# Optimization experiments

Measured on AMD Instinct MI355X. Metric: run time of the kernel, lower is better.

## Reference

```python
import jax, jax.numpy as jnp
import numpy as np

N_NODES = 50000
N_EDGES = 800000
N_GRAPHS = 500
DIM = 64
RBF_DIM = 5      # ceil(cutoff/width) = ceil(5.0/1)
N_CONV = 3
N_TYPES = 100
CLS_DIM = 2000
CUTOFF = 5.0

def _w(key, shape, fan_in):
    return jax.random.normal(key, shape, dtype=jnp.float32) / np.sqrt(fan_in)

def setup_inputs() -> dict:
    key = jax.random.key(0)
    ks = jax.random.split(key, 16)
    return {
        "node_types": jax.random.randint(ks[0], (N_NODES,), 0, N_TYPES, dtype=jnp.int32),
        "edge_src": jax.random.randint(ks[1], (N_EDGES,), 0, N_NODES, dtype=jnp.int32),
        "edge_dst": jax.random.randint(ks[2], (N_EDGES,), 0, N_NODES, dtype=jnp.int32),
        "graph_ids": jnp.sort(jax.random.randint(ks[3], (N_NODES,), 0, N_GRAPHS, dtype=jnp.int32)),
        "distance": jax.random.uniform(ks[4], (N_EDGES,), dtype=jnp.float32) * CUTOFF,
        "emb": jax.random.normal(ks[5], (N_TYPES, DIM), dtype=jnp.float32),
        "conv_w1": _w(ks[6], (N_CONV, DIM, DIM), DIM),
        "cf1_w": _w(ks[7], (N_CONV, RBF_DIM, DIM), RBF_DIM),
        "cf1_b": jnp.zeros((N_CONV, DIM), jnp.float32),
        "cf2_w": _w(ks[8], (N_CONV, DIM, DIM), DIM),
        "cf2_b": jnp.zeros((N_CONV, DIM), jnp.float32),
        "nl2_w": _w(ks[9], (N_CONV, DIM, DIM), DIM),
        "nl2_b": jnp.zeros((N_CONV, DIM), jnp.float32),
        "nl3_w": _w(ks[10], (N_CONV, DIM, DIM), DIM),
        "nl3_b": jnp.zeros((N_CONV, DIM), jnp.float32),
        "d1_w": _w(ks[11], (DIM, 256), DIM),
        "d1_b": jnp.zeros((256,), jnp.float32),
        "d2_w": _w(ks[12], (256, 256), 256),
        "d2_b": jnp.zeros((256,), jnp.float32),
        "cls_w": _w(ks[13], (256, CLS_DIM), 256),
        "cls_b": jnp.zeros((CLS_DIM,), jnp.float32),
        "ac_w": _w(ks[14], (256, N_TYPES), 256),
        "ac_b": jnp.zeros((N_TYPES,), jnp.float32),
    }

def _sp2(x):
    # torch nn.Softplus(beta=0.5): (1/0.5) * log(1 + exp(0.5 * x))
    return 2.0 * jax.nn.softplus(0.5 * x)

def reference(node_types, edge_src, edge_dst, graph_ids, distance, emb,
              conv_w1, cf1_w, cf1_b, cf2_w, cf2_b, nl2_w, nl2_b, nl3_w, nl3_b,
              d1_w, d1_b, d2_w, d2_b, cls_w, cls_b, ac_w, ac_b):
    # RBF expansion of edge distances: centers = linspace(low, high, n_centers)
    centers = jnp.linspace(0.0, CUTOFF, RBF_DIM)
    gap = centers[1] - centers[0]
    rbf = jnp.exp(-(1.0 / gap) * (distance[:, None] - centers) ** 2)  # [E, RBF_DIM]

    node = emb[node_types]                                            # AtomEmbedding -> [N, D]
    for i in range(N_CONV):                                           # Interaction layers
        new_node = node @ conv_w1[i]                                  # Linear(dim, dim, bias=False)
        eh = _sp2(rbf @ cf1_w[i] + cf1_b[i])                          # CFConv filter network
        eh = _sp2(eh @ cf2_w[i] + cf2_b[i])                           # [E, D]
        msg = new_node[edge_src] * eh                                 # fn.u_mul_e gather
        agg = jax.ops.segment_sum(msg, edge_dst, num_segments=N_NODES)  # fn.sum scatter
        t = _sp2(agg @ nl2_w[i] + nl2_b[i])
        node = node + t @ nl3_w[i] + nl3_b[i]                         # residual update

    atom = node @ d1_w + d1_b
    atom = jax.nn.softplus(atom) - jnp.log(2.0)                       # ShiftSoftplus
    res = atom @ d2_w + d2_b                                          # [N, 256]
    atoms_preds = jax.nn.relu(res) @ ac_w + ac_b                      # [N, 100]

    ones = jnp.ones((N_NODES,), jnp.float32)
    counts = jax.ops.segment_sum(ones, graph_ids, num_segments=N_GRAPHS)
    emb_g = jax.ops.segment_sum(res, graph_ids, num_segments=N_GRAPHS) / jnp.maximum(counts, 1.0)[:, None]
    cls_preds = emb_g @ cls_w + cls_b                                 # [B, cls_dim]
    return atoms_preds, cls_preds
```

## Files before the change

kernel.cpp:

```cpp
#include <hip/hip_runtime.h>
#include <math.h>

#define N_NODES 50000
#define N_EDGES 800000
#define N_GRAPHS 500
#define DIM 64
#define RBF_DIM 5
#define N_CONV 3
#define CLS_DIM 2000
#define ACT_DIM 100
#define HID 256
#define TAB 256
#define TABP (TAB - 1)
#define CAP 64

typedef __attribute__((ext_vector_type(8))) short bf16x8;
typedef __attribute__((ext_vector_type(4))) float f32x4;
#define MFMA16(a,b,c) __builtin_amdgcn_mfma_f32_16x16x32_bf16(a,b,c,0,0,0)

__device__ __forceinline__ float sp2f(float x){
    float y = 0.5f * x;
    return 2.0f * (fmaxf(y, 0.0f) + __logf(1.0f + __expf(-fabsf(y))));
}
__device__ __forceinline__ float sspf(float x){
    return fmaxf(x, 0.0f) + __logf(1.0f + __expf(-fabsf(x))) - 0.69314718055994531f;
}
__device__ __forceinline__ short f2b(float x){
    union { float f; unsigned u; } v; v.f = x;
    unsigned r = v.u + 0x7FFFu + ((v.u >> 16) & 1u);
    return (short)(r >> 16);
}
__device__ __forceinline__ float b2f(short x){
    union { unsigned u; float f; } v; v.u = ((unsigned)(unsigned short)x) << 16;
    return v.f;
}

__global__ void k_tw(const float* __restrict__ cw, const float* __restrict__ n2,
                     const float* __restrict__ n3, const float* __restrict__ d1w,
                     const float* __restrict__ d2w, const float* __restrict__ acw,
                     const float* __restrict__ clsw, const float* __restrict__ emb,
                     short* __restrict__ cwt, short* __restrict__ n2t, short* __restrict__ n3t,
                     short* __restrict__ d1t, short* __restrict__ d2t, short* __restrict__ act,
                     short* __restrict__ clswt, short* __restrict__ embw0b){
    int b = blockIdx.x, tid = threadIdx.x;
    if (b < 144){
        int i = b * 256 + tid;
        int y = i >> 12, j = i & 4095;
        int which = y / 3, layer = y % 3;
        const float* src = (which == 0 ? cw : which == 1 ? n2 : n3) + layer * 4096;
        short* dst = (which == 0 ? cwt : which == 1 ? n2t : n3t) + layer * 4096;
        int k = j >> 6, n = j & 63;
        dst[n * 64 + k] = f2b(src[k * 64 + n]);
    } else if (b < 208){
        int i = (b - 144) * 256 + tid;
        int k = i >> 8, n = i & 255;
        d1t[n * 64 + k] = f2b(d1w[k * 256 + n]);
    } else if (b < 464){
        int i = (b - 208) * 256 + tid;
        int k = i >> 8, n = i & 255;
        d2t[n * 256 + k] = f2b(d2w[k * 256 + n]);
    } else if (b < 576){
        int i = (b - 464) * 256 + tid;
        int n = i >> 8, k = i & 255;
        act[n * 256 + k] = f2b(n < ACT_DIM ? acw[k * ACT_DIM + n] : 0.f);
    } else if (b < 2624){
        int i = (b - 576) * 256 + tid;
        int k = i >> 11, n = i & 2047;
        clswt[n * 256 + k] = f2b(n < CLS_DIM ? clsw[k * CLS_DIM + n] : 0.f);
    } else {
        int i = (b - 2624) * 256 + tid;
        if (i < 100 * 64){
            int t = i >> 6, c = i & 63;
            float a = 0.f;
            #pragma unroll 8
            for (int k = 0; k < 64; ++k) a += emb[t * 64 + k] * cw[k * 64 + c];
            embw0b[i] = f2b(a);
        }
    }
}

__global__ void k_embed(const int* __restrict__ types, const float* __restrict__ emb,
                        const short* __restrict__ embw0b,
                        float* __restrict__ node, short* __restrict__ nodeb,
                        short* __restrict__ nnb,
                        const int* __restrict__ gid, float* __restrict__ counts){
    int i = blockIdx.x * 256 + threadIdx.x;
    if (i < N_NODES * DIM){
        int t = types[i >> 6], c = i & 63;
        float v = emb[t * 64 + c];
        node[i] = v; nodeb[i] = f2b(v);
        nnb[i] = embw0b[t * 64 + c];
    }
    if (i < N_NODES) atomicAdd(&counts[gid[i]], 1.0f);
}

__global__ void k_scat(const int* __restrict__ esrc, const int* __restrict__ edst,
                       const float* __restrict__ dist,
                       int* __restrict__ cnt, unsigned* __restrict__ edata){
    int e = blockIdx.x * 256 + threadIdx.x;
    if (e >= N_EDGES) return;
    int d = edst[e];
    int pos = atomicAdd(&cnt[d], 1);
    if (pos < CAP){
        const float SC16 = (float)(TAB - 1) * 16.0f / 5.0f;
        int v = (int)(dist[e] * SC16 + 0.5f);
        v = min(v, (TAB - 1) * 16);
        edata[d * CAP + pos] = ((unsigned)v << 17) | (unsigned)esrc[e];
    }
}

__global__ __launch_bounds__(256) void k_table3(const float* __restrict__ cf1w_all,
    const float* __restrict__ cf1b_all, const float* __restrict__ cf2w_all,
    const float* __restrict__ cf2b_all, unsigned* __restrict__ tabp_all)
{
    int L = blockIdx.y;
    const float* cf1w = cf1w_all + L * RBF_DIM * DIM;
    const float* cf1b = cf1b_all + L * DIM;
    const float* cf2w = cf2w_all + L * DIM * DIM;
    const float* cf2b = cf2b_all + L * DIM;
    unsigned short* tp = (unsigned short*)(tabp_all + L * TABP * 64);
    __shared__ float s_cf1[RBF_DIM * 64];
    __shared__ float s_cf1b[64], s_cf2b[64];
    __shared__ float s_cf2[64 * 64];
    __shared__ float s_h1[4 * 64];
    int tid = threadIdx.x;
    int c = tid & 63, g = tid >> 6;
    for (int i = tid; i < 64 * 64; i += 256) s_cf2[i] = cf2w[i];
    for (int i = tid; i < RBF_DIM * 64; i += 256) s_cf1[i] = cf1w[i];
    if (tid < 64){ s_cf1b[tid] = cf1b[tid]; s_cf2b[tid] = cf2b[tid]; }
    __syncthreads();
    int entry = blockIdx.x * 4 + g;
    float d = (float)entry * (5.0f / (float)(TAB - 1));
    {
        float acc = s_cf1b[c];
        #pragma unroll
        for (int j = 0; j < RBF_DIM; ++j){
            float t = d - 1.25f * (float)j;
            acc += __expf(-0.8f * t * t) * s_cf1[j * 64 + c];
        }
        s_h1[g * 64 + c] = sp2f(acc);
    }
    __syncthreads();
    {
        float acc = s_cf2b[c];
        #pragma unroll 8
        for (int k = 0; k < 64; ++k) acc += s_h1[g * 64 + k] * s_cf2[k * 64 + c];
        unsigned short h = (unsigned short)f2b(sp2f(acc));
        if (entry < TABP) tp[(entry * 64 + c) * 2] = h;
        if (entry > 0)    tp[((entry - 1) * 64 + c) * 2 + 1] = h;
    }
}

__global__ __launch_bounds__(256) void k_agg(const unsigned* __restrict__ edata,
    const int* __restrict__ cnt, const unsigned* __restrict__ tabp,
    const short* __restrict__ nnb, short* __restrict__ aggb)
{
    int tid = threadIdx.x;
    int c = tid & 63, r = tid >> 6;
    int n = blockIdx.x * 4 + r;
    if (n >= N_NODES) return;
    int m = min(cnt[n], CAP);
    unsigned ev = (c < m) ? edata[n * CAP + c] : 0u;
    int s_l = (int)(ev & 0x1FFFFu);
    int v_l = (int)(ev >> 17);
    int i0_l = min(v_l >> 4, TAB - 2);
    float f_l = (float)(v_l - (i0_l << 4)) * 0.0625f;
    int pk_l = (i0_l << 17) | s_l;
    float acc = 0.f;
    int e = 0;
    for (; e + 8 <= m; e += 8){
        int p[8]; float f[8];
        #pragma unroll
        for (int j = 0; j < 8; ++j){ p[j] = __shfl(pk_l, e + j); f[j] = __shfl(f_l, e + j); }
        unsigned u[8]; float nn[8];
        #pragma unroll
        for (int j = 0; j < 8; ++j){
            u[j]  = tabp[(p[j] >> 17) * 64 + c];
            nn[j] = b2f(nnb[(p[j] & 0x1FFFF) * 64 + c]);
        }
        #pragma unroll
        for (int j = 0; j < 8; ++j){
            float w0 = __uint_as_float(u[j] << 16);
            float w1 = __uint_as_float(u[j] & 0xffff0000u);
            acc += nn[j] * (w0 + (w1 - w0) * f[j]);
        }
    }
    for (; e + 4 <= m; e += 4){
        int p[4]; float f[4];
        #pragma unroll
        for (int j = 0; j < 4; ++j){ p[j] = __shfl(pk_l, e + j); f[j] = __shfl(f_l, e + j); }
        unsigned u[4]; float nn[4];
        #pragma unroll
        for (int j = 0; j < 4; ++j){
            u[j]  = tabp[(p[j] >> 17) * 64 + c];
            nn[j] = b2f(nnb[(p[j] & 0x1FFFF) * 64 + c]);
        }
        #pragma unroll
        for (int j = 0; j < 4; ++j){
            float w0 = __uint_as_float(u[j] << 16);
            float w1 = __uint_as_float(u[j] & 0xffff0000u);
            acc += nn[j] * (w0 + (w1 - w0) * f[j]);
        }
    }
    for (; e < m; ++e){
        int   p = __shfl(pk_l, e); float f = __shfl(f_l, e);
        int i0 = p >> 17, s = p & 0x1FFFF;
        unsigned u = tabp[i0 * 64 + c];
        float w0 = __uint_as_float(u << 16), w1 = __uint_as_float(u & 0xffff0000u);
        acc += b2f(nnb[s * 64 + c]) * (w0 + (w1 - w0) * f);
    }
    aggb[n * 64 + c] = f2b(acc);
}

__global__ __launch_bounds__(256) void k_update(const short* __restrict__ aggb,
    const short* __restrict__ nl2t, const float* __restrict__ nl2b,
    const short* __restrict__ nl3t, const float* __restrict__ nl3b,
    float* __restrict__ node, short* __restrict__ nodeb,
    const short* __restrict__ wnext, short* __restrict__ nnb)
{
    __shared__ short sT[32 * 80];
    int tid = threadIdx.x, wave = tid >> 6, lane = tid & 63;
    int quad = lane >> 4, l16 = lane & 15;
    int row0 = blockIdx.x * 32;
    int rt = wave >> 1;
    int ctb = (wave & 1) * 2;
    f32x4 acc[2] = {{0,0,0,0},{0,0,0,0}};
    #pragma unroll
    for (int kt = 0; kt < 2; ++kt){
        int k0 = kt * 32 + quad * 8;
        int rw = row0 + rt * 16 + l16;
        bf16x8 a = (rw < N_NODES) ? *(const bf16x8*)&aggb[rw * 64 + k0] : (bf16x8){0,0,0,0,0,0,0,0};
        #pragma unroll
        for (int i = 0; i < 2; ++i){
            bf16x8 b = *(const bf16x8*)&nl2t[((ctb + i) * 16 + l16) * 64 + k0];
            acc[i] = MFMA16(a, b, acc[i]);
        }
    }
    #pragma unroll
    for (int i = 0; i < 2; ++i)
        #pragma unroll
        for (int reg = 0; reg < 4; ++reg){
            int rl = rt * 16 + quad * 4 + reg;
            int col = (ctb + i) * 16 + l16;
            sT[rl * 80 + col] = f2b(sp2f(acc[i][reg] + nl2b[col]));
        }
    __syncthreads();
    f32x4 acc2[2] = {{0,0,0,0},{0,0,0,0}};
    #pragma unroll
    for (int kt = 0; kt < 2; ++kt){
        int k0 = kt * 32 + quad * 8;
        bf16x8 a = *(const bf16x8*)&sT[(rt * 16 + l16) * 80 + k0];
        #pragma unroll
        for (int i = 0; i < 2; ++i){
            bf16x8 b = *(const bf16x8*)&nl3t[((ctb + i) * 16 + l16) * 64 + k0];
            acc2[i] = MFMA16(a, b, acc2[i]);
        }
    }
    short vb[2][4];
    #pragma unroll
    for (int i = 0; i < 2; ++i)
        #pragma unroll
        for (int reg = 0; reg < 4; ++reg){
            int row = row0 + rt * 16 + quad * 4 + reg;
            int col = (ctb + i) * 16 + l16;
            float v = 0.f;
            if (row < N_NODES){
                v = node[row * 64 + col] + acc2[i][reg] + nl3b[col];
                node[row * 64 + col] = v;
            }
            short vbs = f2b(v);
            vb[i][reg] = vbs;
            if (row < N_NODES) nodeb[row * 64 + col] = vbs;
        }
    if (wnext){
        __syncthreads();
        #pragma unroll
        for (int i = 0; i < 2; ++i)
            #pragma unroll
            for (int reg = 0; reg < 4; ++reg)
                sT[(rt * 16 + quad * 4 + reg) * 80 + (ctb + i) * 16 + l16] = vb[i][reg];
        __syncthreads();
        f32x4 acc3[2] = {{0,0,0,0},{0,0,0,0}};
        #pragma unroll
        for (int kt = 0; kt < 2; ++kt){
            int k0 = kt * 32 + quad * 8;
            bf16x8 a = *(const bf16x8*)&sT[(rt * 16 + l16) * 80 + k0];
            #pragma unroll
            for (int i = 0; i < 2; ++i){
                bf16x8 b = *(const bf16x8*)&wnext[((ctb + i) * 16 + l16) * 64 + k0];
                acc3[i] = MFMA16(a, b, acc3[i]);
            }
        }
        #pragma unroll
        for (int i = 0; i < 2; ++i)
            #pragma unroll
            for (int reg = 0; reg < 4; ++reg){
                int row = row0 + rt * 16 + quad * 4 + reg;
                int col = (ctb + i) * 16 + l16;
                if (row < N_NODES) nnb[row * 64 + col] = f2b(acc3[i][reg]);
            }
    }
}

__global__ __launch_bounds__(256) void k_r123(const short* __restrict__ nodeb,
    const short* __restrict__ d1t, const float* __restrict__ d1b,
    const short* __restrict__ d2t, const float* __restrict__ d2b_,
    const short* __restrict__ act, const float* __restrict__ acb,
    const int* __restrict__ gid, float* __restrict__ gacc,
    float* __restrict__ out_atoms)
{
    __shared__ short satom[32 * 264];
    int tid = threadIdx.x, wave = tid >> 6, lane = tid & 63;
    int quad = lane >> 4, l16 = lane & 15;
    int row0 = blockIdx.x * 32;
    {
        f32x4 acc[2][4] = {{{0,0,0,0},{0,0,0,0},{0,0,0,0},{0,0,0,0}},
                           {{0,0,0,0},{0,0,0,0},{0,0,0,0},{0,0,0,0}}};
        #pragma unroll
        for (int kt = 0; kt < 2; ++kt){
            int k0 = kt * 32 + quad * 8;
            bf16x8 a[2];
            #pragma unroll
            for (int rt = 0; rt < 2; ++rt){
                int rw = row0 + rt * 16 + l16;
                a[rt] = (rw < N_NODES) ? *(const bf16x8*)&nodeb[rw * 64 + k0] : (bf16x8){0,0,0,0,0,0,0,0};
            }
            #pragma unroll
            for (int ct = 0; ct < 4; ++ct){
                bf16x8 b = *(const bf16x8*)&d1t[(wave * 64 + ct * 16 + l16) * 64 + k0];
                #pragma unroll
                for (int rt = 0; rt < 2; ++rt) acc[rt][ct] = MFMA16(a[rt], b, acc[rt][ct]);
            }
        }
        #pragma unroll
        for (int rt = 0; rt < 2; ++rt)
            #pragma unroll
            for (int ct = 0; ct < 4; ++ct){
                int col = wave * 64 + ct * 16 + l16;
                float bb = d1b[col];
                #pragma unroll
                for (int reg = 0; reg < 4; ++reg)
                    satom[(rt * 16 + quad * 4 + reg) * 264 + col] = f2b(sspf(acc[rt][ct][reg] + bb));
            }
    }
    __syncthreads();
    f32x4 acc2[2][4] = {{{0,0,0,0},{0,0,0,0},{0,0,0,0},{0,0,0,0}},
                        {{0,0,0,0},{0,0,0,0},{0,0,0,0},{0,0,0,0}}};
    for (int kt = 0; kt < 8; ++kt){
        int k0 = kt * 32 + quad * 8;
        bf16x8 a[2];
        #pragma unroll
        for (int rt = 0; rt < 2; ++rt)
            a[rt] = *(const bf16x8*)&satom[(rt * 16 + l16) * 264 + k0];
        #pragma unroll
        for (int ct = 0; ct < 4; ++ct){
            bf16x8 b = *(const bf16x8*)&d2t[(wave * 64 + ct * 16 + l16) * HID + k0];
            #pragma unroll
            for (int rt = 0; rt < 2; ++rt) acc2[rt][ct] = MFMA16(a[rt], b, acc2[rt][ct]);
        }
    }
    __syncthreads();
    #pragma unroll
    for (int rt = 0; rt < 2; ++rt)
        #pragma unroll
        for (int ct = 0; ct < 4; ++ct){
            int col = wave * 64 + ct * 16 + l16;
            float bb = d2b_[col];
            #pragma unroll
            for (int reg = 0; reg < 4; ++reg)
                satom[(rt * 16 + quad * 4 + reg) * 264 + col] = f2b(acc2[rt][ct][reg] + bb);
        }
    __syncthreads();
    {
        float run[4] = {0.f, 0.f, 0.f, 0.f};
        int   cur[4] = {-1, -1, -1, -1};
        for (int r = 0; r < 8; ++r){
            #pragma unroll
            for (int ch = 0; ch < 4; ++ch){
                int row = ch * 8 + r;
                int n = row0 + row;
                if (n >= N_NODES) continue;
                short s = satom[row * 264 + tid];
                float v = b2f(s);
                int g = gid[n];
                if (g != cur[ch]){
                    if (cur[ch] >= 0) atomicAdd(&gacc[cur[ch] * HID + tid], run[ch]);
                    run[ch] = 0.f; cur[ch] = g;
                }
                run[ch] += v;
                satom[row * 264 + tid] = (v > 0.f) ? s : (short)0;
            }
        }
        #pragma unroll
        for (int ch = 0; ch < 4; ++ch)
            if (cur[ch] >= 0) atomicAdd(&gacc[cur[ch] * HID + tid], run[ch]);
    }
    __syncthreads();
    {
        int nct = (wave < 3) ? 2 : 1;
        f32x4 acc3[2][2] = {{{0,0,0,0},{0,0,0,0}},{{0,0,0,0},{0,0,0,0}}};
        for (int kt = 0; kt < 8; ++kt){
            int k0 = kt * 32 + quad * 8;
            bf16x8 a[2];
            #pragma unroll
            for (int rt = 0; rt < 2; ++rt)
                a[rt] = *(const bf16x8*)&satom[(rt * 16 + l16) * 264 + k0];
            for (int j = 0; j < nct; ++j){
                int ct = wave + j * 4;
                bf16x8 b = *(const bf16x8*)&act[(ct * 16 + l16) * HID + k0];
                #pragma unroll
                for (int rt = 0; rt < 2; ++rt) acc3[rt][j] = MFMA16(a[rt], b, acc3[rt][j]);
            }
        }
        #pragma unroll
        for (int rt = 0; rt < 2; ++rt)
            for (int j = 0; j < nct; ++j){
                int col = (wave + j * 4) * 16 + l16;
                if (col >= ACT_DIM) continue;
                float bb = acb[col];
                #pragma unroll
                for (int reg = 0; reg < 4; ++reg){
                    int row = row0 + rt * 16 + quad * 4 + reg;
                    if (row < N_NODES) out_atoms[row * ACT_DIM + col] = acc3[rt][j][reg] + bb;
                }
            }
    }
}

__global__ void k_embg(const float* __restrict__ gacc, const float* __restrict__ counts,
                       short* __restrict__ gclsb){
    int i = blockIdx.x * 256 + threadIdx.x;
    if (i < N_GRAPHS * HID){
        int g = i >> 8;
        gclsb[i] = f2b(gacc[i] / fmaxf(counts[g], 1.0f));
    }
}

__global__ __launch_bounds__(256) void k_cls2(const short* __restrict__ gclsb,
    const short* __restrict__ clswt, const float* __restrict__ clsb,
    float* __restrict__ out_cls)
{
    int tid = threadIdx.x, wave = tid >> 6, lane = tid & 63;
    int quad = lane >> 4, l16 = lane & 15;
    int row0 = blockIdx.x * 32;
    int colbase = blockIdx.y * 256 + wave * 64;
    f32x4 acc[2][4] = {{{0,0,0,0},{0,0,0,0},{0,0,0,0},{0,0,0,0}},
                       {{0,0,0,0},{0,0,0,0},{0,0,0,0},{0,0,0,0}}};
    for (int kt = 0; kt < 8; ++kt){
        int k0 = kt * 32 + quad * 8;
        bf16x8 a[2];
        #pragma unroll
        for (int rt = 0; rt < 2; ++rt){
            int rw = row0 + rt * 16 + l16;
            a[rt] = (rw < N_GRAPHS) ? *(const bf16x8*)&gclsb[rw * HID + k0] : (bf16x8){0,0,0,0,0,0,0,0};
        }
        #pragma unroll
        for (int ct = 0; ct < 4; ++ct){
            bf16x8 b = *(const bf16x8*)&clswt[(colbase + ct * 16 + l16) * HID + k0];
            #pragma unroll
            for (int rt = 0; rt < 2; ++rt) acc[rt][ct] = MFMA16(a[rt], b, acc[rt][ct]);
        }
    }
    #pragma unroll
    for (int rt = 0; rt < 2; ++rt)
        #pragma unroll
        for (int ct = 0; ct < 4; ++ct){
            int col = colbase + ct * 16 + l16;
            if (col >= CLS_DIM) continue;
            float bb = clsb[col];
            #pragma unroll
            for (int reg = 0; reg < 4; ++reg){
                int row = row0 + rt * 16 + quad * 4 + reg;
                if (row < N_GRAPHS) out_cls[row * CLS_DIM + col] = acc[rt][ct][reg] + bb;
            }
        }
}

extern "C" void kernel_launch(void* const* d_in, const int* in_sizes, int n_in,
                              void* d_out, int out_size, void* d_ws, size_t ws_size,
                              hipStream_t stream)
{
    const int*   node_types = (const int*)d_in[0];
    const int*   edge_src   = (const int*)d_in[1];
    const int*   edge_dst   = (const int*)d_in[2];
    const int*   graph_ids  = (const int*)d_in[3];
    const float* distance   = (const float*)d_in[4];
    const float* emb        = (const float*)d_in[5];
    const float* conv_w1    = (const float*)d_in[6];
    const float* cf1_w      = (const float*)d_in[7];
    const float* cf1_b      = (const float*)d_in[8];
    const float* cf2_w      = (const float*)d_in[9];
    const float* cf2_b      = (const float*)d_in[10];
    const float* nl2_w      = (const float*)d_in[11];
    const float* nl2_b      = (const float*)d_in[12];
    const float* nl3_w      = (const float*)d_in[13];
    const float* nl3_b      = (const float*)d_in[14];
    const float* d1_w       = (const float*)d_in[15];
    const float* d1_b       = (const float*)d_in[16];
    const float* d2_w       = (const float*)d_in[17];
    const float* d2_b       = (const float*)d_in[18];
    const float* cls_w      = (const float*)d_in[19];
    const float* cls_b      = (const float*)d_in[20];
    const float* ac_w       = (const float*)d_in[21];
    const float* ac_b       = (const float*)d_in[22];

    float*    gacc   = (float*)d_ws;
    float*    counts = gacc + 128000;
    int*      cnt    = (int*)(counts + 512);
    short*    nodeb  = (short*)(cnt + 50048);
    short*    nnb    = nodeb + 3200000;
    short*    aggb   = nnb + 3200000;
    unsigned* tabp   = (unsigned*)(aggb + 3200000);
    short*    cw1t   = (short*)(tabp + 3 * 16320);
    short*    n2t    = cw1t + 12288;
    short*    n3t    = n2t + 12288;
    short*    d1t    = n3t + 12288;
    short*    d2t    = d1t + 16384;
    short*    act    = d2t + 65536;
    short*    clswt  = act + 28672;
    short*    gclsb  = clswt + 524288;
    short*    embw0b = gclsb + 128000;
    float*    node   = (float*)(embw0b + 6400);
    unsigned* edata  = (unsigned*)(node + 3200000);
    float*    out    = (float*)d_out;

    (void)hipMemsetAsync(gacc, 0, (128000 + 512) * sizeof(float) + 50048 * sizeof(int), stream);

    k_tw<<<2649, 256, 0, stream>>>(conv_w1, nl2_w, nl3_w, d1_w, d2_w, ac_w, cls_w, emb,
                                   cw1t, n2t, n3t, d1t, d2t, act, clswt, embw0b);
    k_table3<<<dim3(TAB / 4, 3), 256, 0, stream>>>(cf1_w, cf1_b, cf2_w, cf2_b, tabp);

    k_embed<<<(N_NODES * DIM + 255) / 256, 256, 0, stream>>>(node_types, emb, embw0b,
        node, nodeb, nnb, graph_ids, counts);
    k_scat<<<(N_EDGES + 255) / 256, 256, 0, stream>>>(edge_src, edge_dst, distance,
                                                      cnt, edata);

    for (int i = 0; i < N_CONV; ++i){
        k_agg<<<(N_NODES + 3) / 4, 256, 0, stream>>>(edata, cnt, tabp + i * TABP * 64,
                                                     nnb, aggb);
        k_update<<<(N_NODES + 31) / 32, 256, 0, stream>>>(aggb,
            n2t + i * 4096, nl2_b + i * DIM, n3t + i * 4096, nl3_b + i * DIM,
            node, nodeb, (i < N_CONV - 1) ? (cw1t + (i + 1) * 4096) : (const short*)nullptr, nnb);
    }

    k_r123<<<(N_NODES + 31) / 32, 256, 0, stream>>>(nodeb, d1t, d1_b, d2t, d2_b,
                                                    act, ac_b, graph_ids, gacc, out);
    k_embg<<<(N_GRAPHS * HID + 255) / 256, 256, 0, stream>>>(gacc, counts, gclsb);
    k_cls2<<<dim3((N_GRAPHS + 31) / 32, (CLS_DIM + 255) / 256), 256, 0, stream>>>(
        gclsb, clswt, cls_b, out + N_NODES * ACT_DIM);
}
```

Measured before the change: 429.5 us.

## Fuse edge aggregation into node update kernel with ping-pong node buffers

Merges the per-node gather/aggregate kernel into the MFMA update kernel. Each 256-thread block now aggregates 32 nodes, with each wave handling 8 nodes one after another, and stages the bf16 aggregates in shared memory instead of a global buffer. The projected node features are double-buffered so the next layer's inputs are not overwritten while other blocks still read them. This removes a launch per layer and the global write and read of the aggregate array. In exchange, each wave now handles nodes serially, which reduces the parallelism available for hiding the latency of the random gather.

New measurement: 432.0 us. About the same (+0.6%).

```diff
diff --git a/kernel.cpp b/kernel.cpp
--- a/kernel.cpp
+++ b/kernel.cpp
@@ -151,85 +151,83 @@
     }
 }
 
-__global__ __launch_bounds__(256) void k_agg(const unsigned* __restrict__ edata,
+__global__ __launch_bounds__(256) void k_conv(const unsigned* __restrict__ edata,
     const int* __restrict__ cnt, const unsigned* __restrict__ tabp,
-    const short* __restrict__ nnb, short* __restrict__ aggb)
-{
-    int tid = threadIdx.x;
-    int c = tid & 63, r = tid >> 6;
-    int n = blockIdx.x * 4 + r;
-    if (n >= N_NODES) return;
-    int m = min(cnt[n], CAP);
-    unsigned ev = (c < m) ? edata[n * CAP + c] : 0u;
-    int s_l = (int)(ev & 0x1FFFFu);
-    int v_l = (int)(ev >> 17);
-    int i0_l = min(v_l >> 4, TAB - 2);
-    float f_l = (float)(v_l - (i0_l << 4)) * 0.0625f;
-    int pk_l = (i0_l << 17) | s_l;
-    float acc = 0.f;
-    int e = 0;
-    for (; e + 8 <= m; e += 8){
-        int p[8]; float f[8];
-        #pragma unroll
-        for (int j = 0; j < 8; ++j){ p[j] = __shfl(pk_l, e + j); f[j] = __shfl(f_l, e + j); }
-        unsigned u[8]; float nn[8];
-        #pragma unroll
-        for (int j = 0; j < 8; ++j){
-            u[j]  = tabp[(p[j] >> 17) * 64 + c];
-            nn[j] = b2f(nnb[(p[j] & 0x1FFFF) * 64 + c]);
-        }
-        #pragma unroll
-        for (int j = 0; j < 8; ++j){
-            float w0 = __uint_as_float(u[j] << 16);
-            float w1 = __uint_as_float(u[j] & 0xffff0000u);
-            acc += nn[j] * (w0 + (w1 - w0) * f[j]);
-        }
-    }
-    for (; e + 4 <= m; e += 4){
-        int p[4]; float f[4];
-        #pragma unroll
-        for (int j = 0; j < 4; ++j){ p[j] = __shfl(pk_l, e + j); f[j] = __shfl(f_l, e + j); }
-        unsigned u[4]; float nn[4];
-        #pragma unroll
-        for (int j = 0; j < 4; ++j){
-            u[j]  = tabp[(p[j] >> 17) * 64 + c];
-            nn[j] = b2f(nnb[(p[j] & 0x1FFFF) * 64 + c]);
-        }
-        #pragma unroll
-        for (int j = 0; j < 4; ++j){
-            float w0 = __uint_as_float(u[j] << 16);
-            float w1 = __uint_as_float(u[j] & 0xffff0000u);
-            acc += nn[j] * (w0 + (w1 - w0) * f[j]);
-        }
-    }
-    for (; e < m; ++e){
-        int   p = __shfl(pk_l, e); float f = __shfl(f_l, e);
-        int i0 = p >> 17, s = p & 0x1FFFF;
-        unsigned u = tabp[i0 * 64 + c];
-        float w0 = __uint_as_float(u << 16), w1 = __uint_as_float(u & 0xffff0000u);
-        acc += b2f(nnb[s * 64 + c]) * (w0 + (w1 - w0) * f);
-    }
-    aggb[n * 64 + c] = f2b(acc);
-}
-
-__global__ __launch_bounds__(256) void k_update(const short* __restrict__ aggb,
+    const short* __restrict__ nnb_in,
     const short* __restrict__ nl2t, const float* __restrict__ nl2b,
     const short* __restrict__ nl3t, const float* __restrict__ nl3b,
     float* __restrict__ node, short* __restrict__ nodeb,
-    const short* __restrict__ wnext, short* __restrict__ nnb)
+    const short* __restrict__ wnext, short* __restrict__ nnb_out)
 {
+    __shared__ short sAgg[32 * 72];
     __shared__ short sT[32 * 80];
     int tid = threadIdx.x, wave = tid >> 6, lane = tid & 63;
     int quad = lane >> 4, l16 = lane & 15;
     int row0 = blockIdx.x * 32;
+    for (int i = 0; i < 8; ++i){
+        int nl = wave * 8 + i;
+        int n = row0 + nl;
+        int c = lane;
+        float acc = 0.f;
+        int m = (n < N_NODES) ? min(cnt[n], CAP) : 0;
+        unsigned ev = (c < m) ? edata[n * CAP + c] : 0u;
+        int s_l = (int)(ev & 0x1FFFFu);
+        int v_l = (int)(ev >> 17);
+        int i0_l = min(v_l >> 4, TAB - 2);
+        float f_l = (float)(v_l - (i0_l << 4)) * 0.0625f;
+        int pk_l = (i0_l << 17) | s_l;
+        int e = 0;
+        for (; e + 8 <= m; e += 8){
+            int p[8]; float f[8];
+            #pragma unroll
+            for (int j = 0; j < 8; ++j){ p[j] = __shfl(pk_l, e + j); f[j] = __shfl(f_l, e + j); }
+            unsigned u[8]; float nn[8];
+            #pragma unroll
+            for (int j = 0; j < 8; ++j){
+                u[j]  = tabp[(p[j] >> 17) * 64 + c];
+                nn[j] = b2f(nnb_in[(p[j] & 0x1FFFF) * 64 + c]);
+            }
+            #pragma unroll
+            for (int j = 0; j < 8; ++j){
+                float w0 = __uint_as_float(u[j] << 16);
+                float w1 = __uint_as_float(u[j] & 0xffff0000u);
+                acc += nn[j] * (w0 + (w1 - w0) * f[j]);
+            }
+        }
+        for (; e + 4 <= m; e += 4){
+            int p[4]; float f[4];
+            #pragma unroll
+            for (int j = 0; j < 4; ++j){ p[j] = __shfl(pk_l, e + j); f[j] = __shfl(f_l, e + j); }
+            unsigned u[4]; float nn[4];
+            #pragma unroll
+            for (int j = 0; j < 4; ++j){
+                u[j]  = tabp[(p[j] >> 17) * 64 + c];
+                nn[j] = b2f(nnb_in[(p[j] & 0x1FFFF) * 64 + c]);
+            }
+            #pragma unroll
+            for (int j = 0; j < 4; ++j){
+                float w0 = __uint_as_float(u[j] << 16);
+                float w1 = __uint_as_float(u[j] & 0xffff0000u);
+                acc += nn[j] * (w0 + (w1 - w0) * f[j]);
+            }
+        }
+        for (; e < m; ++e){
+            int   p = __shfl(pk_l, e); float f = __shfl(f_l, e);
+            int i0 = p >> 17, s = p & 0x1FFFF;
+            unsigned u = tabp[i0 * 64 + c];
+            float w0 = __uint_as_float(u << 16), w1 = __uint_as_float(u & 0xffff0000u);
+            acc += b2f(nnb_in[s * 64 + c]) * (w0 + (w1 - w0) * f);
+        }
+        sAgg[nl * 72 + c] = f2b(acc);
+    }
+    __syncthreads();
     int rt = wave >> 1;
     int ctb = (wave & 1) * 2;
     f32x4 acc[2] = {{0,0,0,0},{0,0,0,0}};
     #pragma unroll
     for (int kt = 0; kt < 2; ++kt){
         int k0 = kt * 32 + quad * 8;
-        int rw = row0 + rt * 16 + l16;
-        bf16x8 a = (rw < N_NODES) ? *(const bf16x8*)&aggb[rw * 64 + k0] : (bf16x8){0,0,0,0,0,0,0,0};
+        bf16x8 a = *(const bf16x8*)&sAgg[(rt * 16 + l16) * 72 + k0];
         #pragma unroll
         for (int i = 0; i < 2; ++i){
             bf16x8 b = *(const bf16x8*)&nl2t[((ctb + i) * 16 + l16) * 64 + k0];
@@ -297,7 +295,7 @@
             for (int reg = 0; reg < 4; ++reg){
                 int row = row0 + rt * 16 + quad * 4 + reg;
                 int col = (ctb + i) * 16 + l16;
-                if (row < N_NODES) nnb[row * 64 + col] = f2b(acc3[i][reg]);
+                if (row < N_NODES) nnb_out[row * 64 + col] = f2b(acc3[i][reg]);
             }
     }
 }
@@ -508,9 +506,9 @@
     float*    counts = gacc + 128000;
     int*      cnt    = (int*)(counts + 512);
     short*    nodeb  = (short*)(cnt + 50048);
-    short*    nnb    = nodeb + 3200000;
-    short*    aggb   = nnb + 3200000;
-    unsigned* tabp   = (unsigned*)(aggb + 3200000);
+    short*    nnb0   = nodeb + 3200000;
+    short*    nnb1   = nnb0 + 3200000;
+    unsigned* tabp   = (unsigned*)(nnb1 + 3200000);
     short*    cw1t   = (short*)(tabp + 3 * 16320);
     short*    n2t    = cw1t + 12288;
     short*    n3t    = n2t + 12288;
@@ -531,16 +529,17 @@
     k_table3<<<dim3(TAB / 4, 3), 256, 0, stream>>>(cf1_w, cf1_b, cf2_w, cf2_b, tabp);
 
     k_embed<<<(N_NODES * DIM + 255) / 256, 256, 0, stream>>>(node_types, emb, embw0b,
-        node, nodeb, nnb, graph_ids, counts);
+        node, nodeb, nnb0, graph_ids, counts);
     k_scat<<<(N_EDGES + 255) / 256, 256, 0, stream>>>(edge_src, edge_dst, distance,
                                                       cnt, edata);
 
     for (int i = 0; i < N_CONV; ++i){
-        k_agg<<<(N_NODES + 3) / 4, 256, 0, stream>>>(edata, cnt, tabp + i * TABP * 64,
-                                                     nnb, aggb);
-        k_update<<<(N_NODES + 31) / 32, 256, 0, stream>>>(aggb,
-            n2t + i * 4096, nl2_b + i * DIM, n3t + i * 4096, nl3_b + i * DIM,
-            node, nodeb, (i < N_CONV - 1) ? (cw1t + (i + 1) * 4096) : (const short*)nullptr, nnb);
+        const short* nin  = (i & 1) ? nnb1 : nnb0;
+        short*       nout = (i & 1) ? nnb0 : nnb1;
+        k_conv<<<(N_NODES + 31) / 32, 256, 0, stream>>>(edata, cnt, tabp + i * TABP * 64,
+            nin, n2t + i * 4096, nl2_b + i * DIM, n3t + i * 4096, nl3_b + i * DIM,
+            node, nodeb,
+            (i < N_CONV - 1) ? (cw1t + (i + 1) * 4096) : (const short*)nullptr, nout);
     }
 
     k_r123<<<(N_NODES + 31) / 32, 256, 0, stream>>>(nodeb, d1t, d1_b, d2t, d2_b,
```
